# Performance work log

Measured on AMD Instinct MI355X. Metric: run time of the kernel, lower is better.

## Reference

```python
import jax, jax.numpy as jnp
import numpy as np

B, N, NB, C, CZ = 4, 1024, 32, 384, 128
EPS = 1e-6


def setup_inputs() -> dict:
    key = jax.random.key(0)
    k1, k2, k3, k4, k5 = jax.random.split(key, 5)
    s_i = jax.random.normal(k1, (B, N, C), dtype=jnp.float32)
    s_ij = jax.random.normal(k2, (B, N, NB, C), dtype=jnp.float32)
    m_ij = jnp.ones((B, N, NB), dtype=jnp.float32)
    z_ij = jax.random.normal(k3, (B, N, NB, CZ), dtype=jnp.float32)
    W_s = jax.random.normal(k4, (C, C), dtype=jnp.float32) / np.sqrt(C)
    W_z = jax.random.normal(k5, (CZ, C), dtype=jnp.float32) / np.sqrt(CZ)
    gamma = jnp.ones((C,), dtype=jnp.float32)
    beta = jnp.zeros((C,), dtype=jnp.float32)
    return {"s_i": s_i, "s_ij": s_ij, "m_ij": m_ij, "z_ij": z_ij,
            "W_s": W_s, "W_z": W_z, "gamma": gamma, "beta": beta}


def reference(s_i, s_ij, m_ij, z_ij, W_s, W_z, gamma, beta):
    # Dense projection of neighbor single act: (B,N,n,C) @ (C,C)
    s_proj = jnp.einsum('bnkc,cd->bnkd', s_ij, W_s)
    # subtract center single act
    diff = s_proj - s_i[..., None, :]
    # gate by projected pair act: (B,N,n,Cz) @ (Cz,C)
    gate = jnp.einsum('bnkz,zd->bnkd', z_ij, W_z)
    msg = diff * gate
    # masked sum over neighbor axis
    s_new = jnp.sum(msg * m_ij[..., None], axis=-2)  # (B,N,C)
    # layernorm over last axis
    mu = jnp.mean(s_new, axis=-1, keepdims=True)
    var = jnp.mean(jnp.square(s_new - mu), axis=-1, keepdims=True)
    s_new = (s_new - mu) * jax.lax.rsqrt(var + EPS) * gamma + beta
    return s_new
```

## Files before the change

kernel.cpp:

```cpp
#include <hip/hip_runtime.h>
#include <hip/hip_bf16.h>

#define B_ 4
#define N_ 1024
#define NB_ 32
#define C_ 384
#define CZ_ 128
#define NSITES (B_ * N_)
#define EPSV 1e-6f
#define SPB 2
#define THREADS 512
#define WCHUNK_B 24576
#define NKS 12
#define NKZ 4

typedef unsigned short u16;
typedef unsigned int u32;
typedef __bf16 bf16x8 __attribute__((ext_vector_type(8)));
typedef float f32x4 __attribute__((ext_vector_type(4)));

__device__ __forceinline__ u16 f2bf(float f) {
    return __builtin_bit_cast(u16, __float2bfloat16(f));
}
__device__ __forceinline__ u32 pk2(float lo, float hi) {
    return ((u32)f2bf(hi) << 16) | f2bf(lo);
}
__device__ __forceinline__ float bfbits2f(u16 u) {
    union { float f; u32 i; } x;
    x.i = ((u32)u) << 16;
    return x.f;
}
__device__ __forceinline__ bf16x8 mk8(float4 lo, float4 hi) {
    union { u32 u[4]; bf16x8 v; } x;
    x.u[0] = pk2(lo.x, lo.y); x.u[1] = pk2(lo.z, lo.w);
    x.u[2] = pk2(hi.x, hi.y); x.u[3] = pk2(hi.z, hi.w);
    return x.v;
}

__global__ void prep_weights(const float* __restrict__ Ws, const float* __restrict__ Wz,
                             u16* __restrict__ wsS, u16* __restrict__ wsZ) {
    int idx = blockIdx.x * 256 + threadIdx.x;
    const int NS = NKS * 4 * C_ * 8;
    if (idx < NS) {
        int e = idx & 7, t = idx >> 3;
        int d = t % C_, u = t / C_;
        int q = u & 3, c = u >> 2;
        int k = c * 32 + q * 8 + e;
        wsS[idx] = f2bf(Ws[k * C_ + d]);
    } else {
        int j = idx - NS;
        if (j < NKZ * 4 * C_ * 8) {
            int e = j & 7, t = j >> 3;
            int d = t % C_, u = t / C_;
            int q = u & 3, c = u >> 2;
            int k = c * 32 + q * 8 + e;
            wsZ[j] = f2bf(Wz[k * C_ + d]);
        }
    }
}

__global__ __launch_bounds__(THREADS, 4)
void fused_msg_kernel(const float* __restrict__ s_i,
                      const float* __restrict__ s_ij,
                      const float* __restrict__ m_ij,
                      const float* __restrict__ z_ij,
                      const u16* __restrict__ wsS,
                      const u16* __restrict__ wsZ,
                      const float* __restrict__ gamma,
                      const float* __restrict__ beta,
                      float* __restrict__ out) {
    __shared__ u16 ldsW[2][WCHUNK_B / 2];
    __shared__ float lds_snew[SPB * C_];

    const int tid = threadIdx.x;
    const int wave = tid >> 6;
    const int lane = tid & 63;
    const int q = lane >> 4;
    const int ln = lane & 15;
    const int mg = wave >> 2;
    const int cb = (wave & 3) * 96;

    const int site0 = blockIdx.x * SPB;
    const long rowbase = (long)site0 * NB_;
    const long arow0 = rowbase + mg * 32 + ln;

    const float mv = m_ij[rowbase + lane];

    const f32x4 ZERO = {0.f, 0.f, 0.f, 0.f};
    f32x4 acc[2][6];
    #pragma unroll
    for (int mt = 0; mt < 2; ++mt)
        #pragma unroll
        for (int nt = 0; nt < 6; ++nt)
            acc[mt][nt] = ZERO;

    float4 ra[2][4];
    const int ldsq = q * (C_ * 8);

#define STAGE_W(wsbase, c, buf) do {                                          \
        const char* _s = (const char*)(wsbase) + (c) * WCHUNK_B;              \
        char* _d = (char*)&ldsW[(buf)][0];                                    \
        _Pragma("unroll")                                                     \
        for (int _i = 0; _i < 3; ++_i) {                                      \
            int _o = _i * 8192 + tid * 16;                                    \
            __builtin_amdgcn_global_load_lds(                                 \
                (const __attribute__((address_space(1))) void*)(_s + _o),     \
                (__attribute__((address_space(3))) void*)(_d + _o),           \
                16, 0, 0);                                                    \
        }                                                                     \
    } while (0)

#define LOAD_A(base, kd, c, sl) do {                                          \
        const float* _p0 = (base) + arow0 * (kd) + (c) * 32 + q * 8;          \
        const float* _p1 = _p0 + 16 * (kd);                                   \
        ra[sl][0] = *reinterpret_cast<const float4*>(_p0);                    \
        ra[sl][1] = *reinterpret_cast<const float4*>(_p0 + 4);                \
        ra[sl][2] = *reinterpret_cast<const float4*>(_p1);                    \
        ra[sl][3] = *reinterpret_cast<const float4*>(_p1 + 4);                \
    } while (0)

#define COMPUTE(sl) do {                                                      \
        bf16x8 _a0 = mk8(ra[sl][0], ra[sl][1]);                               \
        bf16x8 _a1 = mk8(ra[sl][2], ra[sl][3]);                               \
        const u16* _lw = &ldsW[sl][ldsq];                                     \
        _Pragma("unroll")                                                     \
        for (int _nt = 0; _nt < 6; ++_nt) {                                   \
            bf16x8 _b = *reinterpret_cast<const bf16x8*>(                     \
                _lw + (cb + _nt * 16 + ln) * 8);                              \
            acc[0][_nt] = __builtin_amdgcn_mfma_f32_16x16x32_bf16(            \
                _a0, _b, acc[0][_nt], 0, 0, 0);                               \
            acc[1][_nt] = __builtin_amdgcn_mfma_f32_16x16x32_bf16(            \
                _a1, _b, acc[1][_nt], 0, 0, 0);                               \
        }                                                                     \
    } while (0)

    STAGE_W(wsZ, 0, 0);
    LOAD_A(z_ij, CZ_, 0, 0);
    __syncthreads();
    #pragma unroll
    for (int c = 0; c < NKZ; ++c) {
        if (c + 1 < NKZ) {
            STAGE_W(wsZ, c + 1, (c + 1) & 1);
            LOAD_A(z_ij, CZ_, c + 1, (c + 1) & 1);
        }
        COMPUTE(c & 1);
        __syncthreads();
    }

    STAGE_W(wsS, 0, 0);
    LOAD_A(s_ij, C_, 0, 0);

    u32 gateb[2][6][2];
    #pragma unroll
    for (int mt = 0; mt < 2; ++mt) {
        int rb = mg * 32 + mt * 16 + q * 4;
        float m0 = __shfl(mv, rb + 0, 64);
        float m1 = __shfl(mv, rb + 1, 64);
        float m2 = __shfl(mv, rb + 2, 64);
        float m3 = __shfl(mv, rb + 3, 64);
        #pragma unroll
        for (int nt = 0; nt < 6; ++nt) {
            gateb[mt][nt][0] = pk2(acc[mt][nt][0] * m0, acc[mt][nt][1] * m1);
            gateb[mt][nt][1] = pk2(acc[mt][nt][2] * m2, acc[mt][nt][3] * m3);
            acc[mt][nt] = ZERO;
        }
    }
    __syncthreads();

    #pragma unroll
    for (int c = 0; c < NKS; ++c) {
        if (c + 1 < NKS) {
            STAGE_W(wsS, c + 1, (c + 1) & 1);
            LOAD_A(s_ij, C_, c + 1, (c + 1) & 1);
        }
        COMPUTE(c & 1);
        __syncthreads();
    }

#undef STAGE_W
#undef LOAD_A
#undef COMPUTE

    #pragma unroll
    for (int nt = 0; nt < 6; ++nt) {
        int col = cb + nt * 16 + ln;
        float si = s_i[(long)(site0 + mg) * C_ + col];
        float p = 0.f;
        #pragma unroll
        for (int mt = 0; mt < 2; ++mt) {
            #pragma unroll
            for (int r = 0; r < 4; ++r) {
                float g = bfbits2f((u16)(gateb[mt][nt][r >> 1] >> ((r & 1) * 16)));
                p += (acc[mt][nt][r] - si) * g;
            }
        }
        p += __shfl_xor(p, 16, 64);
        p += __shfl_xor(p, 32, 64);
        if (q == 0) lds_snew[mg * C_ + col] = p;
    }
    __syncthreads();

    if (wave < SPB) {
        const int site = wave;
        float v[6];
        float sum = 0.f, sumsq = 0.f;
        #pragma unroll
        for (int i = 0; i < 6; ++i) {
            v[i] = lds_snew[site * C_ + lane + i * 64];
            sum += v[i];
            sumsq += v[i] * v[i];
        }
        #pragma unroll
        for (int off = 32; off >= 1; off >>= 1) {
            sum += __shfl_xor(sum, off, 64);
            sumsq += __shfl_xor(sumsq, off, 64);
        }
        float mu = sum * (1.f / C_);
        float var = sumsq * (1.f / C_) - mu * mu;
        float rs = rsqrtf(var + EPSV);
        #pragma unroll
        for (int i = 0; i < 6; ++i) {
            int col = lane + i * 64;
            out[(long)(site0 + site) * C_ + col] = (v[i] - mu) * rs * gamma[col] + beta[col];
        }
    }
}

extern "C" void kernel_launch(void* const* d_in, const int* in_sizes, int n_in,
                              void* d_out, int out_size, void* d_ws, size_t ws_size,
                              hipStream_t stream) {
    (void)in_sizes; (void)n_in; (void)out_size; (void)ws_size;
    const float* s_i   = (const float*)d_in[0];
    const float* s_ij  = (const float*)d_in[1];
    const float* m_ij  = (const float*)d_in[2];
    const float* z_ij  = (const float*)d_in[3];
    const float* W_s   = (const float*)d_in[4];
    const float* W_z   = (const float*)d_in[5];
    const float* gamma = (const float*)d_in[6];
    const float* beta  = (const float*)d_in[7];
    float* out = (float*)d_out;

    u16* wsS = (u16*)d_ws;
    u16* wsZ = wsS + NKS * 4 * C_ * 8;

    int prep_elems = NKS * 4 * C_ * 8 + NKZ * 4 * C_ * 8;
    prep_weights<<<(prep_elems + 255) / 256, 256, 0, stream>>>(W_s, W_z, wsS, wsZ);
    fused_msg_kernel<<<NSITES / SPB, THREADS, 0, stream>>>(s_i, s_ij, m_ij, z_ij,
                                                           wsS, wsZ, gamma, beta, out);
}
```

Before: 468.1 us.

## Merge gate and projection K-loops into one triple-buffered pipeline with partial waits

Fuses the z-gate GEMM loop and the s projection loop into a single 16-chunk loop with three LDS/register buffers and a prefetch distance of two chunks. Full __syncthreads are replaced by explicit s_waitcnt vmcnt(7) plus s_barrier, so the next chunk's loads stay in flight while the current chunk computes. This also removes the pipeline drain and refill between the two GEMM phases. The cost is extra LDS (3x24KB) and extra registers for the third A buffer, which may reduce occupancy at 4 blocks per CU. The correctness of the hand-counted vmcnt depends on the exact number of outstanding loads per chunk.

```diff
diff --git a/kernel.cpp b/kernel.cpp
--- a/kernel.cpp
+++ b/kernel.cpp
@@ -11,8 +11,9 @@
 #define SPB 2
 #define THREADS 512
 #define WCHUNK_B 24576
+#define NKZ 4
 #define NKS 12
-#define NKZ 4
+#define NCH (NKZ + NKS)
 
 typedef unsigned short u16;
 typedef unsigned int u32;
@@ -69,7 +70,7 @@
                       const float* __restrict__ gamma,
                       const float* __restrict__ beta,
                       float* __restrict__ out) {
-    __shared__ u16 ldsW[2][WCHUNK_B / 2];
+    __shared__ u16 ldsW[3][WCHUNK_B / 2];
     __shared__ float lds_snew[SPB * C_];
 
     const int tid = threadIdx.x;
@@ -94,12 +95,18 @@
         for (int nt = 0; nt < 6; ++nt)
             acc[mt][nt] = ZERO;
 
-    float4 ra[2][4];
+    float4 ra[3][4];
+    u32 gateb[2][6][2];
     const int ldsq = q * (C_ * 8);
 
-#define STAGE_W(wsbase, c, buf) do {                                          \
-        const char* _s = (const char*)(wsbase) + (c) * WCHUNK_B;              \
-        char* _d = (char*)&ldsW[(buf)][0];                                    \
+#define CH_A(cc)  ((cc) < NKZ ? z_ij : s_ij)
+#define CH_KD(cc) ((cc) < NKZ ? CZ_ : C_)
+#define CH_CK(cc) ((cc) < NKZ ? (cc) : (cc) - NKZ)
+#define CH_W(cc)  ((cc) < NKZ ? wsZ : wsS)
+
+#define STAGE(cc) do {                                                        \
+        const char* _s = (const char*)CH_W(cc) + CH_CK(cc) * WCHUNK_B;        \
+        char* _d = (char*)&ldsW[(cc) % 3][0];                                 \
         _Pragma("unroll")                                                     \
         for (int _i = 0; _i < 3; ++_i) {                                      \
             int _o = _i * 8192 + tid * 16;                                    \
@@ -110,19 +117,19 @@
         }                                                                     \
     } while (0)
 
-#define LOAD_A(base, kd, c, sl) do {                                          \
-        const float* _p0 = (base) + arow0 * (kd) + (c) * 32 + q * 8;          \
-        const float* _p1 = _p0 + 16 * (kd);                                   \
-        ra[sl][0] = *reinterpret_cast<const float4*>(_p0);                    \
-        ra[sl][1] = *reinterpret_cast<const float4*>(_p0 + 4);                \
-        ra[sl][2] = *reinterpret_cast<const float4*>(_p1);                    \
-        ra[sl][3] = *reinterpret_cast<const float4*>(_p1 + 4);                \
+#define LOADA(cc) do {                                                        \
+        const float* _p0 = CH_A(cc) + arow0 * CH_KD(cc) + CH_CK(cc) * 32 + q * 8; \
+        const float* _p1 = _p0 + 16 * CH_KD(cc);                              \
+        ra[(cc) % 3][0] = *reinterpret_cast<const float4*>(_p0);              \
+        ra[(cc) % 3][1] = *reinterpret_cast<const float4*>(_p0 + 4);          \
+        ra[(cc) % 3][2] = *reinterpret_cast<const float4*>(_p1);              \
+        ra[(cc) % 3][3] = *reinterpret_cast<const float4*>(_p1 + 4);          \
     } while (0)
 
-#define COMPUTE(sl) do {                                                      \
-        bf16x8 _a0 = mk8(ra[sl][0], ra[sl][1]);                               \
-        bf16x8 _a1 = mk8(ra[sl][2], ra[sl][3]);                               \
-        const u16* _lw = &ldsW[sl][ldsq];                                     \
+#define COMPUTE(cc) do {                                                      \
+        bf16x8 _a0 = mk8(ra[(cc) % 3][0], ra[(cc) % 3][1]);                   \
+        bf16x8 _a1 = mk8(ra[(cc) % 3][2], ra[(cc) % 3][3]);                   \
+        const u16* _lw = &ldsW[(cc) % 3][ldsq];                               \
         _Pragma("unroll")                                                     \
         for (int _nt = 0; _nt < 6; ++_nt) {                                   \
             bf16x8 _b = *reinterpret_cast<const bf16x8*>(                     \
@@ -134,52 +141,53 @@
         }                                                                     \
     } while (0)
 
-    STAGE_W(wsZ, 0, 0);
-    LOAD_A(z_ij, CZ_, 0, 0);
-    __syncthreads();
+    STAGE(0); LOADA(0);
+    STAGE(1); LOADA(1);
+    asm volatile("s_waitcnt vmcnt(7)" ::: "memory");
+    __builtin_amdgcn_s_barrier();
+    __builtin_amdgcn_sched_barrier(0);
+
     #pragma unroll
-    for (int c = 0; c < NKZ; ++c) {
-        if (c + 1 < NKZ) {
-            STAGE_W(wsZ, c + 1, (c + 1) & 1);
-            LOAD_A(z_ij, CZ_, c + 1, (c + 1) & 1);
-        }
-        COMPUTE(c & 1);
-        __syncthreads();
-    }
-
-    STAGE_W(wsS, 0, 0);
-    LOAD_A(s_ij, C_, 0, 0);
-
-    u32 gateb[2][6][2];
-    #pragma unroll
-    for (int mt = 0; mt < 2; ++mt) {
-        int rb = mg * 32 + mt * 16 + q * 4;
-        float m0 = __shfl(mv, rb + 0, 64);
-        float m1 = __shfl(mv, rb + 1, 64);
-        float m2 = __shfl(mv, rb + 2, 64);
-        float m3 = __shfl(mv, rb + 3, 64);
-        #pragma unroll
-        for (int nt = 0; nt < 6; ++nt) {
-            gateb[mt][nt][0] = pk2(acc[mt][nt][0] * m0, acc[mt][nt][1] * m1);
-            gateb[mt][nt][1] = pk2(acc[mt][nt][2] * m2, acc[mt][nt][3] * m3);
-            acc[mt][nt] = ZERO;
-        }
-    }
-    __syncthreads();
-
-    #pragma unroll
-    for (int c = 0; c < NKS; ++c) {
-        if (c + 1 < NKS) {
-            STAGE_W(wsS, c + 1, (c + 1) & 1);
-            LOAD_A(s_ij, C_, c + 1, (c + 1) & 1);
-        }
-        COMPUTE(c & 1);
-        __syncthreads();
-    }
-
-#undef STAGE_W
-#undef LOAD_A
+    for (int c = 0; c < NCH; ++c) {
+        if (c + 2 < NCH) { STAGE(c + 2); LOADA(c + 2); }
+
+        COMPUTE(c);
+
+        if (c == NKZ - 1) {
+            #pragma unroll
+            for (int mt = 0; mt < 2; ++mt) {
+                int rb = mg * 32 + mt * 16 + q * 4;
+                float m0 = __shfl(mv, rb + 0, 64);
+                float m1 = __shfl(mv, rb + 1, 64);
+                float m2 = __shfl(mv, rb + 2, 64);
+                float m3 = __shfl(mv, rb + 3, 64);
+                #pragma unroll
+                for (int nt = 0; nt < 6; ++nt) {
+                    gateb[mt][nt][0] = pk2(acc[mt][nt][0] * m0, acc[mt][nt][1] * m1);
+                    gateb[mt][nt][1] = pk2(acc[mt][nt][2] * m2, acc[mt][nt][3] * m3);
+                    acc[mt][nt] = ZERO;
+                }
+            }
+        }
+
+        if (c + 1 < NCH) {
+            if (c + 2 < NCH) {
+                asm volatile("s_waitcnt vmcnt(7)" ::: "memory");
+            } else {
+                asm volatile("s_waitcnt vmcnt(0)" ::: "memory");
+            }
+            __builtin_amdgcn_s_barrier();
+            __builtin_amdgcn_sched_barrier(0);
+        }
+    }
+
+#undef STAGE
+#undef LOADA
 #undef COMPUTE
+#undef CH_A
+#undef CH_KD
+#undef CH_CK
+#undef CH_W
 
     #pragma unroll
     for (int nt = 0; nt < 6; ++nt) {
```

New measurement: 491.7 us. +5.0%, slower.
